# Optimization experiments

Measured on AMD Instinct MI355X. Metric: run time of the kernel, lower is better.

The kernel has to match this reference:

```python
import math
import jax, jax.numpy as jnp
import numpy as np

N_LAYER = 6
THETA = 2.0 ** 16
LN_EPS = 1e-5


def _ln(x):
    # LayerNorm over last dim, no affine (elementwise_affine=False)
    mu = x.mean(-1, keepdims=True)
    var = ((x - mu) ** 2).mean(-1, keepdims=True)
    return (x - mu) / jnp.sqrt(var + LN_EPS)


def _rope(phases, v):
    # phases: (T, N); v: (B, H, T, N)
    ph = (phases % 1.0) * (2.0 * math.pi)
    c, s = jnp.cos(ph), jnp.sin(ph)
    v2 = v.reshape(v.shape[:-1] + (-1, 2))
    v_rot = jnp.stack((-v2[..., 1], v2[..., 0]), axis=-1).reshape(v.shape)
    return v * c + v_rot * s


def setup_inputs() -> dict:
    key = jax.random.key(0)
    ks = jax.random.split(key, 6)
    B, T, D, nh, mult, V = 2, 512, 256, 4, 64, 256
    N = D * mult // nh  # 4096 neurons per head
    std = 0.02
    return {
        "input_ids": jax.random.randint(ks[0], (B, T), 0, V, dtype=jnp.int64),
        "embed_table": jax.random.normal(ks[1], (V, D), jnp.float32) * std,
        "encoder": jax.random.normal(ks[2], (nh, D, N), jnp.float32) * std,
        "encoder_v": jax.random.normal(ks[3], (nh, D, N), jnp.float32) * std,
        "decoder": jax.random.normal(ks[4], (nh * N, D), jnp.float32) * std,
        "lm_head": jax.random.normal(ks[5], (D, V), jnp.float32) * std,
    }


def reference(input_ids, embed_table, encoder, encoder_v, decoder, lm_head):
    B, T = input_ids.shape
    nh, D, N = encoder.shape
    # RoPE freqs: quantize(arange(N), 2) / N exponent (matches get_freqs)
    qidx = jnp.floor(jnp.arange(N, dtype=jnp.float32) / 2.0) * 2.0
    freqs = 1.0 / (THETA ** (qidx / N)) / (2.0 * math.pi)
    phases = jnp.arange(T, dtype=jnp.float32)[:, None] * freqs[None, :]  # (T, N)
    # strictly-lower causal mask (tril with diagonal=-1)
    causal = jnp.tril(jnp.ones((T, T), dtype=bool), k=-1)
    dec = decoder.reshape(nh, N, D)  # head-major, matches transpose(1,2).reshape

    x = _ln(embed_table[input_ids])[:, None]  # (B, 1, T, D)
    trace = None
    for _ in range(N_LAYER):  # shared (tied) weights across layers
        x_sparse = jax.nn.relu(jnp.einsum('bitd,hdn->bhtn', x, encoder))  # (B,H,T,N)
        qr = _rope(phases, x_sparse)
        scores = jnp.einsum('bhtn,bhsn->bhts', qr, qr)  # linear attn, no softmax
        scores = jnp.where(causal, scores, 0.0)
        ykv = _ln(jnp.einsum('bhts,bisd->bhtd', scores, x))  # (B,H,T,D)
        y_sparse = jax.nn.relu(jnp.einsum('bhtd,hdn->bhtn', ykv, encoder_v))
        xy_sparse = x_sparse * y_sparse  # elementwise gate
        trace = xy_sparse  # keep only last layer (used for neuron_trace)
        ymlp = jnp.einsum('bhtn,hnd->btd', xy_sparse, dec)[:, None]  # (B,1,T,D)
        x = _ln(x + _ln(ymlp))

    xs = x[:, 0]  # (B, T, D)
    logits = xs @ lm_head  # (B, T, V)
    embedding = xs.mean(axis=1)  # (B, D), pool_output, no mask
    neuron_trace = trace.mean(axis=2).reshape(B, -1)  # (B, H*N)
    return logits, embedding, neuron_trace
```

## Files before the change

kernel.cpp:

```cpp
#include <hip/hip_runtime.h>
#include <hip/hip_bf16.h>
#include <hip/hip_fp16.h>

#define TT 512
#define DD 256
#define NH 4
#define NN 4096
#define VV 256
#define NLAYER 6
#define BB 2
#define BH (BB * NH)
#define NPAIR 2048

typedef __attribute__((ext_vector_type(8))) short bf16x8;
typedef __attribute__((ext_vector_type(4))) float f32x4;
typedef __attribute__((ext_vector_type(8))) unsigned short us8;
typedef __attribute__((ext_vector_type(4))) unsigned short us4;

#define AS1 __attribute__((address_space(1)))
#define AS3 __attribute__((address_space(3)))

__device__ __forceinline__ void glds16(const unsigned short* g, unsigned short* l) {
  __builtin_amdgcn_global_load_lds((const AS1 void*)g, (AS3 void*)l, 16, 0, 0);
}

__device__ __forceinline__ unsigned short f2bf(float f) {
  unsigned int u = __float_as_uint(f);
  return (unsigned short)((u + 0x7FFFu + ((u >> 16) & 1u)) >> 16);
}
__device__ __forceinline__ float bf2f(unsigned short h) {
  return __uint_as_float((unsigned int)h << 16);
}
__device__ __forceinline__ float h2f(unsigned short h) {
  __half x = *reinterpret_cast<__half*>(&h);
  return __half2float(x);
}

__device__ __forceinline__ float block_sum_256(float v) {
  __shared__ float s[4];
  #pragma unroll
  for (int o = 32; o > 0; o >>= 1) v += __shfl_down(v, o);
  int lane = threadIdx.x & 63, wid = threadIdx.x >> 6;
  if (lane == 0) s[wid] = v;
  __syncthreads();
  float r = s[0] + s[1] + s[2] + s[3];
  __syncthreads();
  return r;
}

__device__ __forceinline__ float wave_sum64(float v) {
  #pragma unroll
  for (int o = 32; o > 0; o >>= 1) v += __shfl_xor(v, o);
  return v;
}

__device__ __forceinline__ void mfma_tile128_w32_dbuf(const unsigned short* __restrict__ A, int lda,
                                                      const unsigned short* __restrict__ B, int ldb,
                                                      int K, f32x4 acc[2][8],
                                                      unsigned short* As, unsigned short* Bs) {
  const int tid = threadIdx.x;
  const int lane = tid & 63, wave = tid >> 6;
  const int fm = lane & 15, fq = lane >> 4;
  const int wrow = wave << 5;
  const int lrow = lane >> 3;
  const int scol = (((lane & 7) ^ lrow) << 3);
  const unsigned short* gA = A + (size_t)(wave * 8 + lrow) * lda + scol;
  const unsigned short* gB = B + (size_t)(wave * 8 + lrow) * ldb + scol;
  const int lbase = wave * 8 * 64;
  const int swz = (fm & 7) << 4;
  #pragma unroll
  for (int i = 0; i < 4; ++i) {
    glds16(gA + (size_t)(i * 32) * lda, As + lbase + i * 32 * 64);
    glds16(gB + (size_t)(i * 32) * ldb, Bs + lbase + i * 32 * 64);
  }
  __syncthreads();
  int cur = 0;
  for (int k0 = 0; k0 < K; k0 += 64) {
    if (k0 + 64 < K) {
      unsigned short* nA = As + (cur ^ 1) * 8192 + lbase;
      unsigned short* nB = Bs + (cur ^ 1) * 8192 + lbase;
      #pragma unroll
      for (int i = 0; i < 4; ++i) {
        glds16(gA + (k0 + 64) + (size_t)(i * 32) * lda, nA + i * 32 * 64);
        glds16(gB + (k0 + 64) + (size_t)(i * 32) * ldb, nB + i * 32 * 64);
      }
    }
    const char* cA = (const char*)(As + cur * 8192);
    const char* cB = (const char*)(Bs + cur * 8192);
    #pragma unroll
    for (int kk = 0; kk < 2; ++kk) {
      bf16x8 af[2], bfv[8];
      #pragma unroll
      for (int i = 0; i < 2; ++i) {
        const int ra = wrow + i * 16 + fm;
        af[i] = *(const bf16x8*)(cA + ((((ra << 7) + (kk << 6) + (fq << 4))) ^ swz));
      }
      #pragma unroll
      for (int i = 0; i < 8; ++i) {
        const int rb = i * 16 + fm;
        bfv[i] = *(const bf16x8*)(cB + ((((rb << 7) + (kk << 6) + (fq << 4))) ^ swz));
      }
      #pragma unroll
      for (int mi = 0; mi < 2; ++mi)
        #pragma unroll
        for (int ni = 0; ni < 8; ++ni)
          acc[mi][ni] = __builtin_amdgcn_mfma_f32_16x16x32_bf16(af[mi], bfv[ni], acc[mi][ni], 0, 0, 0);
    }
    __syncthreads();
    cur ^= 1;
  }
}

__device__ __forceinline__ void mfma_tile128_dbuf(const unsigned short* __restrict__ A, int lda,
                                                  const unsigned short* __restrict__ B, int ldb,
                                                  int K, f32x4 acc[4][4],
                                                  unsigned short* As, unsigned short* Bs) {
  const int tid = threadIdx.x;
  const int lane = tid & 63, wave = tid >> 6;
  const int fm = lane & 15, fq = lane >> 4;
  const int rw = (wave >> 1) << 6, cw = (wave & 1) << 6;
  const int lrow = lane >> 3;
  const int scol = (((lane & 7) ^ lrow) << 3);
  const unsigned short* gA = A + (size_t)(wave * 8 + lrow) * lda + scol;
  const unsigned short* gB = B + (size_t)(wave * 8 + lrow) * ldb + scol;
  const int lbase = wave * 8 * 64;
  const int swz = (fm & 7) << 4;
  #pragma unroll
  for (int i = 0; i < 4; ++i) {
    glds16(gA + (size_t)(i * 32) * lda, As + lbase + i * 32 * 64);
    glds16(gB + (size_t)(i * 32) * ldb, Bs + lbase + i * 32 * 64);
  }
  __syncthreads();
  int cur = 0;
  for (int k0 = 0; k0 < K; k0 += 64) {
    if (k0 + 64 < K) {
      unsigned short* nA = As + (cur ^ 1) * 8192 + lbase;
      unsigned short* nB = Bs + (cur ^ 1) * 8192 + lbase;
      #pragma unroll
      for (int i = 0; i < 4; ++i) {
        glds16(gA + (k0 + 64) + (size_t)(i * 32) * lda, nA + i * 32 * 64);
        glds16(gB + (k0 + 64) + (size_t)(i * 32) * ldb, nB + i * 32 * 64);
      }
    }
    const char* cA = (const char*)(As + cur * 8192);
    const char* cB = (const char*)(Bs + cur * 8192);
    #pragma unroll
    for (int kk = 0; kk < 2; ++kk) {
      bf16x8 af[4], bfv[4];
      #pragma unroll
      for (int i = 0; i < 4; ++i) {
        const int ra = rw + i * 16 + fm;
        const int rb = cw + i * 16 + fm;
        af[i]  = *(const bf16x8*)(cA + ((((ra << 7) + (kk << 6) + (fq << 4))) ^ swz));
        bfv[i] = *(const bf16x8*)(cB + ((((rb << 7) + (kk << 6) + (fq << 4))) ^ swz));
      }
      #pragma unroll
      for (int mi = 0; mi < 4; ++mi)
        #pragma unroll
        for (int ni = 0; ni < 4; ++ni)
          acc[mi][ni] = __builtin_amdgcn_mfma_f32_16x16x32_bf16(af[mi], bfv[ni], acc[mi][ni], 0, 0, 0);
    }
    __syncthreads();
    cur ^= 1;
  }
}


__global__ __launch_bounds__(256) void k_csinit(unsigned int* __restrict__ cs) {
  int idx = blockIdx.x * 256 + threadIdx.x;
  int t = idx >> 11, p = idx & (NPAIR - 1);
  const float INV2PI = 0.15915494309189535f;
  const float TWOPI = 6.283185307179586f;
  float f = exp2f(-16.0f * (float)(2 * p) / (float)NN) * INV2PI;
  float ph = fmodf((float)t * f, 1.0f) * TWOPI;
  float s, c;
  sincosf(ph, &s, &c);
  __half hc = __float2half_rn(c), hs = __float2half_rn(s);
  unsigned short uc = *reinterpret_cast<unsigned short*>(&hc);
  unsigned short us_ = *reinterpret_cast<unsigned short*>(&hs);
  cs[idx] = ((unsigned int)us_ << 16) | uc;
}

__global__ __launch_bounds__(256) void k_tcast(const float* __restrict__ in,
                                               unsigned short* __restrict__ out,
                                               int R, int C) {
  __shared__ float tile[64][65];
  const size_t zoff = (size_t)blockIdx.z * R * C;
  const int r0 = blockIdx.y * 64, c0 = blockIdx.x * 64;
  const int cl = threadIdx.x & 63, r4 = threadIdx.x >> 6;
  #pragma unroll 4
  for (int i = 0; i < 16; ++i) {
    int rl = r4 * 16 + i;
    tile[rl][cl] = in[zoff + (size_t)(r0 + rl) * C + c0 + cl];
  }
  __syncthreads();
  #pragma unroll 4
  for (int i = 0; i < 16; ++i) {
    int ccl = r4 * 16 + i;
    out[zoff + (size_t)(c0 + ccl) * R + r0 + cl] = f2bf(tile[cl][ccl]);
  }
}

__global__ __launch_bounds__(256) void k_embed_ln(const int* __restrict__ idw,
                                                  const float* __restrict__ tbl,
                                                  float* __restrict__ x,
                                                  unsigned short* __restrict__ xbf,
                                                  unsigned short* __restrict__ xTbf) {
  __shared__ int s_id;
  int row = blockIdx.x, tid = threadIdx.x;
  if (tid == 0) {
    bool is64 = true;
    for (int i = 1; i < 64; i += 2)
      if (idw[i] != 0) { is64 = false; break; }
    s_id = is64 ? idw[2 * row] : idw[row];
  }
  __syncthreads();
  int id = s_id;
  float v = tbl[(size_t)id * DD + tid];
  float mu = block_sum_256(v) * (1.0f / DD);
  float d = v - mu;
  float var = block_sum_256(d * d) * (1.0f / DD);
  float r = d * rsqrtf(var + 1e-5f);
  x[(size_t)row * DD + tid] = r;
  unsigned short rb = f2bf(r);
  xbf[(size_t)row * DD + tid] = rb;
  int b = row >> 9, t = row & 511;
  xTbf[((size_t)b * DD + tid) * TT + t] = rb;
}


__global__ __launch_bounds__(256) void k_enc(const unsigned short* __restrict__ xbf,
                                             const unsigned short* __restrict__ encT,
                                             const unsigned int* __restrict__ csh,
                                             unsigned short* __restrict__ xsp,
                                             unsigned short* __restrict__ qr) {
  __shared__ unsigned short smem[32768];
  unsigned short* As = smem;
  unsigned short* Bs = smem + 16384;
  float* smemf = (float*)smem;
  const int tid = threadIdx.x;
  const int lin = blockIdx.x;
  const int bh = lin & 7, r0 = lin >> 3;
  const int b = bh >> 2, h = bh & 3;
  const int m0 = (r0 >> 5) * 128, n0 = (r0 & 31) * 128;
  f32x4 acc[2][8] = {};
  mfma_tile128_w32_dbuf(xbf + (size_t)b * TT * DD + (size_t)m0 * DD, DD,
                        encT + (size_t)h * NN * DD + (size_t)n0 * DD, DD, DD, acc, As, Bs);
  const int lane = tid & 63, wave = tid >> 6;
  const int fm = lane & 15, fq = lane >> 4;
  float* Scw = smemf + wave * (16 * 132);
  const int rr4 = lane >> 4, c0 = (lane & 15) << 3;
  const size_t base = (size_t)bh * TT * NN;
  #pragma unroll
  for (int mi = 0; mi < 2; ++mi) {
    if (mi) asm volatile("s_waitcnt lgkmcnt(0)" ::: "memory");
    #pragma unroll
    for (int ni = 0; ni < 8; ++ni)
      #pragma unroll
      for (int r = 0; r < 4; ++r)
        Scw[(fq * 4 + r) * 132 + ni * 16 + fm] = acc[mi][ni][r];
    asm volatile("s_waitcnt lgkmcnt(0)" ::: "memory");
    #pragma unroll
    for (int k = 0; k < 4; ++k) {
      const int rr = k * 4 + rr4;
      float v[8];
      *(float4*)&v[0] = *(const float4*)&Scw[rr * 132 + c0];
      *(float4*)&v[4] = *(const float4*)&Scw[rr * 132 + c0 + 4];
      const int t = m0 + wave * 32 + mi * 16 + rr;
      const int n = n0 + c0;
      #pragma unroll
      for (int j = 0; j < 8; ++j) v[j] = fmaxf(v[j], 0.0f);
      us8 o;
      #pragma unroll
      for (int j = 0; j < 8; ++j) o[j] = f2bf(v[j]);
      size_t off = base + (size_t)t * NN + n;
      *(us8*)(xsp + off) = o;
      const unsigned short* cp = (const unsigned short*)(csh + (size_t)t * NPAIR + (n >> 1));
      us8 cv = *(const us8*)cp;
      us8 q;
      #pragma unroll
      for (int j = 0; j < 4; ++j) {
        float c = h2f(cv[2 * j]), s = h2f(cv[2 * j + 1]);
        float ve = v[2 * j], vo = v[2 * j + 1];
        q[2 * j]     = f2bf(ve * c - vo * s);
        q[2 * j + 1] = f2bf(vo * c + ve * s);
      }
      *(us8*)(qr + off) = q;
    }
  }
}

__global__ __launch_bounds__(256) void k_scores_part(const unsigned short* __restrict__ qr,
                                                     float* __restrict__ scp) {
  __shared__ float smemf[16384];
  unsigned short* As = (unsigned short*)smemf;
  unsigned short* Bs = As + 16384;
  const int lin = blockIdx.x;
  const int xcd = lin & 7, slot = lin >> 3;
  const int zg = slot / 10, p = slot - zg * 10;
  const int z = xcd * 4 + zg;
  const int bh = z >> 2, kc = z & 3;
  const int mt = (p > 0) + (p > 2) + (p > 5);
  const int nt = p - mt * (mt + 1) / 2;
  const int m0 = mt * 128, n0 = nt * 128;
  const unsigned short* Q = qr + (size_t)bh * TT * NN + kc * 1024;
  f32x4 acc[4][4] = {};
  mfma_tile128_dbuf(Q + (size_t)m0 * NN, NN, Q + (size_t)n0 * NN, NN, 1024, acc, As, Bs);
  const int lane = threadIdx.x & 63, wave = threadIdx.x >> 6;
  const int fm = lane & 15, fq = lane >> 4;
  const int rw = (wave >> 1) << 6, cw = (wave & 1) << 6;
  float* C = scp + (size_t)z * TT * TT;
  const bool diag = (m0 == n0);
  #pragma unroll
  for (int ni = 0; ni < 4; ++ni) {
    int s = n0 + cw + ni * 16 + fm;
    #pragma unroll
    for (int mi = 0; mi < 4; ++mi) {
      int trow = m0 + rw + mi * 16 + (fq << 2);
      #pragma unroll
      for (int r = 0; r < 4; ++r) {
        float v = acc[mi][ni][r];
        if (diag && s >= trow + r) v = 0.0f;
        C[(size_t)(trow + r) * TT + s] = v;
      }
    }
  }
}

__global__ __launch_bounds__(256) void k_ykv_part(const float* __restrict__ scp,
                                                  const unsigned short* __restrict__ xTbf,
                                                  float* __restrict__ ykvp) {
  __shared__ unsigned short As[64][40];
  __shared__ unsigned short Bs[256][40];
  const int tid = threadIdx.x;
  const int lin = blockIdx.x;
  const int bh = lin & 7, r0 = lin >> 3;
  const int m0 = (r0 & 7) * 64, ks = r0 >> 3, b = bh >> 2;
  if (ks * 128 >= m0 + 64) return;
  float* C = ykvp + ((size_t)(bh * 4 + ks) * TT + m0) * DD;
  const int lane = tid & 63, wave = tid >> 6;
  const int srow = tid >> 2, sk = (tid & 3) << 3;
  const int fm = lane & 15, fq = lane >> 4;
  const int t = m0 + srow;
  const size_t abase0 = (size_t)(bh * 4) * TT * TT + (size_t)t * TT;
  const unsigned short* Brow = xTbf + ((size_t)b * DD + tid) * TT + ks * 128;
  f32x4 acc[16] = {};
  for (int k0 = 0; k0 < 128; k0 += 32) {
    const int s0 = ks * 128 + k0 + sk;
    const float* p = scp + abase0 + s0;
    float sum[8];
    float4 u0 = *(const float4*)(p);
    float4 u1 = *(const float4*)(p + 4);
    sum[0] = u0.x; sum[1] = u0.y; sum[2] = u0.z; sum[3] = u0.w;
    sum[4] = u1.x; sum[5] = u1.y; sum[6] = u1.z; sum[7] = u1.w;
    #pragma unroll
    for (int kc = 1; kc < 4; ++kc) {
      float4 v0 = *(const float4*)(p + (size_t)kc * TT * TT);
      float4 v1 = *(const float4*)(p + (size_t)kc * TT * TT + 4);
      sum[0] += v0.x; sum[1] += v0.y; sum[2] += v0.z; sum[3] += v0.w;
      sum[4] += v1.x; sum[5] += v1.y; sum[6] += v1.z; sum[7] += v1.w;
    }
    us8 av;
    #pragma unroll
    for (int j = 0; j < 8; ++j) av[j] = f2bf(sum[j]);
    us8 bv0 = *(const us8*)(Brow + k0);
    us8 bv1 = *(const us8*)(Brow + k0 + 8);
    us8 bv2 = *(const us8*)(Brow + k0 + 16);
    us8 bv3 = *(const us8*)(Brow + k0 + 24);
    __syncthreads();
    *(us8*)(&As[srow][sk]) = av;
    *(us8*)(&Bs[tid][0]) = bv0;
    *(us8*)(&Bs[tid][8]) = bv1;
    *(us8*)(&Bs[tid][16]) = bv2;
    *(us8*)(&Bs[tid][24]) = bv3;
    __syncthreads();
    bf16x8 a = *(const bf16x8*)(&As[wave * 16 + fm][fq << 3]);
    #pragma unroll
    for (int ni = 0; ni < 16; ++ni) {
      bf16x8 bfr = *(const bf16x8*)(&Bs[ni * 16 + fm][fq << 3]);
      acc[ni] = __builtin_amdgcn_mfma_f32_16x16x32_bf16(a, bfr, acc[ni], 0, 0, 0);
    }
  }
  const int trow = wave * 16 + (fq << 2);
  #pragma unroll
  for (int ni = 0; ni < 16; ++ni)
    #pragma unroll
    for (int r = 0; r < 4; ++r)
      C[(size_t)(trow + r) * DD + ni * 16 + fm] = acc[ni][r];
}

__global__ __launch_bounds__(256) void k_ykv_red(const float* __restrict__ ykvp,
                                                 unsigned short* __restrict__ ykvbf) {
  int row = blockIdx.x * 4 + (threadIdx.x >> 6);
  int lane = threadIdx.x & 63;
  int bh = row >> 9, t = row & 511;
  int d0 = lane << 2;
  int nks = (t >> 7) + 1;
  size_t base = ((size_t)(bh * 4) * TT + t) * DD + d0;
  f32x4 v = *(const f32x4*)(ykvp + base);
  if (nks > 1) v += *(const f32x4*)(ykvp + base + (size_t)TT * DD);
  if (nks > 2) v += *(const f32x4*)(ykvp + base + (size_t)2 * TT * DD);
  if (nks > 3) v += *(const f32x4*)(ykvp + base + (size_t)3 * TT * DD);
  float mu = wave_sum64(v.x + v.y + v.z + v.w) * (1.0f / DD);
  f32x4 d = v - mu;
  float var = wave_sum64(d.x * d.x + d.y * d.y + d.z * d.z + d.w * d.w) * (1.0f / DD);
  f32x4 r = d * rsqrtf(var + 1e-5f);
  us4 rb;
  #pragma unroll
  for (int j = 0; j < 4; ++j) rb[j] = f2bf(r[j]);
  *(us4*)(ykvbf + (size_t)row * DD + d0) = rb;
}

__global__ __launch_bounds__(256) void k_ysp_xy(const unsigned short* __restrict__ ykvbf,
                                                const unsigned short* __restrict__ encvT,
                                                const unsigned short* __restrict__ xsp,
                                                unsigned short* __restrict__ xy) {
  __shared__ unsigned short smem[32768];
  unsigned short* As = smem;
  unsigned short* Bs = smem + 16384;
  float* smemf = (float*)smem;
  const int tid = threadIdx.x;
  const int lin = blockIdx.x;
  const int bh = lin & 7, r0 = lin >> 3;
  const int h = bh & 3;
  const int m0 = (r0 >> 5) * 128, n0 = (r0 & 31) * 128;
  f32x4 acc[2][8] = {};
  mfma_tile128_w32_dbuf(ykvbf + (size_t)bh * TT * DD + (size_t)m0 * DD, DD,
                        encvT + (size_t)h * NN * DD + (size_t)n0 * DD, DD, DD, acc, As, Bs);
  const int lane = tid & 63, wave = tid >> 6;
  const int fm = lane & 15, fq = lane >> 4;
  float* Scw = smemf + wave * (16 * 132);
  const int rr4 = lane >> 4, c0 = (lane & 15) << 3;
  const size_t base = (size_t)bh * TT * NN;
  #pragma unroll
  for (int mi = 0; mi < 2; ++mi) {
    if (mi) asm volatile("s_waitcnt lgkmcnt(0)" ::: "memory");
    #pragma unroll
    for (int ni = 0; ni < 8; ++ni)
      #pragma unroll
      for (int r = 0; r < 4; ++r)
        Scw[(fq * 4 + r) * 132 + ni * 16 + fm] = acc[mi][ni][r];
    asm volatile("s_waitcnt lgkmcnt(0)" ::: "memory");
    #pragma unroll
    for (int k = 0; k < 4; ++k) {
      const int rr = k * 4 + rr4;
      float v[8];
      *(float4*)&v[0] = *(const float4*)&Scw[rr * 132 + c0];
      *(float4*)&v[4] = *(const float4*)&Scw[rr * 132 + c0 + 4];
      const int t = m0 + wave * 32 + mi * 16 + rr;
      const int n = n0 + c0;
      size_t off = base + (size_t)t * NN + n;
      us8 x0 = *(const us8*)(xsp + off);
      us8 o;
      #pragma unroll
      for (int j = 0; j < 8; ++j)
        o[j] = f2bf(bf2f(x0[j]) * fmaxf(v[j], 0.0f));
      *(us8*)(xy + off) = o;
    }
  }
}

__global__ __launch_bounds__(256) void k_ymlp(const unsigned short* __restrict__ xy,
                                              const unsigned short* __restrict__ decT,
                                              float* __restrict__ ym32) {
  __shared__ float smemf[16384];
  unsigned short* As = (unsigned short*)smemf;
  unsigned short* Bs = As + 16384;
  const int lin = blockIdx.x;
  const int xcd = lin & 7, r0 = lin >> 3;
  const int z = xcd * 8 + (r0 >> 3);
  const int tile = r0 & 7;
  const int bh = z >> 3, ks = z & 7, h = bh & 3;
  const int m0 = (tile & 3) * 128, n0 = (tile >> 2) * 128;
  f32x4 acc[4][4] = {};
  mfma_tile128_dbuf(xy + (size_t)bh * TT * NN + (size_t)m0 * NN + ks * 512, NN,
                    decT + (size_t)h * DD * NN + (size_t)n0 * NN + ks * 512, NN,
                    512, acc, As, Bs);
  const int lane = threadIdx.x & 63, wave = threadIdx.x >> 6;
  const int fm = lane & 15, fq = lane >> 4;
  const int rw = (wave >> 1) << 6, cw = (wave & 1) << 6;
  float* C = ym32 + (size_t)z * TT * DD;
  #pragma unroll
  for (int ni = 0; ni < 4; ++ni) {
    int d = n0 + cw + ni * 16 + fm;
    #pragma unroll
    for (int mi = 0; mi < 4; ++mi) {
      int trow = m0 + rw + mi * 16 + (fq << 2);
      #pragma unroll
      for (int r = 0; r < 4; ++r)
        C[(size_t)(trow + r) * DD + d] = acc[mi][ni][r];
    }
  }
}

__global__ __launch_bounds__(256) void k_ln2(float* __restrict__ x,
                                             const float* __restrict__ ym32,
                                             unsigned short* __restrict__ xbf,
                                             unsigned short* __restrict__ xTbf) {
  int row = blockIdx.x * 4 + (threadIdx.x >> 6);
  int lane = threadIdx.x & 63;
  int b = row >> 9, t = row & 511;
  int d0 = lane << 2;
  f32x4 y = {0.0f, 0.0f, 0.0f, 0.0f};
  size_t rbase = (size_t)t * DD + d0;
  #pragma unroll
  for (int p = 0; p < 32; ++p)
    y += *(const f32x4*)(ym32 + (size_t)(b * 32 + p) * TT * DD + rbase);
  float mu = wave_sum64(y.x + y.y + y.z + y.w) * (1.0f / DD);
  f32x4 d = y - mu;
  float var = wave_sum64(d.x * d.x + d.y * d.y + d.z * d.z + d.w * d.w) * (1.0f / DD);
  f32x4 ly = d * rsqrtf(var + 1e-5f);
  f32x4 xv = *(const f32x4*)(x + (size_t)row * DD + d0) + ly;
  float mu2 = wave_sum64(xv.x + xv.y + xv.z + xv.w) * (1.0f / DD);
  f32x4 d2 = xv - mu2;
  float var2 = wave_sum64(d2.x * d2.x + d2.y * d2.y + d2.z * d2.z + d2.w * d2.w) * (1.0f / DD);
  f32x4 r = d2 * rsqrtf(var2 + 1e-5f);
  *(f32x4*)(x + (size_t)row * DD + d0) = r;
  us4 rb;
  #pragma unroll
  for (int j = 0; j < 4; ++j) rb[j] = f2bf(r[j]);
  *(us4*)(xbf + (size_t)row * DD + d0) = rb;
  #pragma unroll
  for (int j = 0; j < 4; ++j)
    xTbf[((size_t)b * DD + d0 + j) * TT + t] = rb[j];
}

__global__ __launch_bounds__(256) void k_trace_part(const unsigned short* __restrict__ xy,
                                                    float* __restrict__ part) {
  const int lin = blockIdx.x;
  const int ts = lin & 7, nc = (lin >> 3) & 1, bh = lin >> 4;
  const int n0 = nc * 2048 + threadIdx.x * 8;
  const size_t base = (size_t)bh * TT * NN + n0;
  float acc[8];
  #pragma unroll
  for (int j = 0; j < 8; ++j) acc[j] = 0.0f;
  for (int t = ts * 64; t < ts * 64 + 64; ++t) {
    us8 v = *(const us8*)(xy + base + (size_t)t * NN);
    #pragma unroll
    for (int j = 0; j < 8; ++j) acc[j] += bf2f(v[j]);
  }
  float* o = part + (size_t)(bh * 8 + ts) * NN + n0;
  #pragma unroll
  for (int j = 0; j < 8; ++j) o[j] = acc[j];
}

__global__ __launch_bounds__(256) void k_trace_red(const float* __restrict__ part,
                                                   float* __restrict__ out) {
  int idx = blockIdx.x * 256 + threadIdx.x;
  int bh = idx >> 12, n = idx & 4095;
  float s = 0.0f;
  #pragma unroll
  for (int ts = 0; ts < 8; ++ts)
    s += part[(size_t)(bh * 8 + ts) * NN + n];
  out[idx] = s * (1.0f / TT);
}

__global__ __launch_bounds__(256) void k_logits(const float* __restrict__ x,
                                                const float* __restrict__ W,
                                                float* __restrict__ out) {
  __shared__ float xs[DD];
  int row = blockIdx.x, tid = threadIdx.x;
  xs[tid] = x[(size_t)row * DD + tid];
  __syncthreads();
  float s = 0.0f;
  #pragma unroll 8
  for (int d = 0; d < DD; ++d) s = fmaf(xs[d], W[(size_t)d * VV + tid], s);
  out[(size_t)row * VV + tid] = s;
}

__global__ __launch_bounds__(256) void k_embedding(const float* __restrict__ x,
                                                   float* __restrict__ out) {
  int idx = blockIdx.x * 256 + threadIdx.x;
  int b = idx >> 8, d = idx & 255;
  float s = 0.0f;
  for (int t = 0; t < TT; ++t) s += x[(size_t)(b * TT + t) * DD + d];
  out[idx] = s * (1.0f / TT);
}

extern "C" void kernel_launch(void* const* d_in, const int* in_sizes, int n_in,
                              void* d_out, int out_size, void* d_ws, size_t ws_size,
                              hipStream_t stream) {
  const int*   ids  = (const int*)d_in[0];
  const float* tbl  = (const float*)d_in[1];
  const float* enc  = (const float*)d_in[2];
  const float* encv = (const float*)d_in[3];
  const float* dec  = (const float*)d_in[4];
  const float* lmh  = (const float*)d_in[5];

  float* ws   = (float*)d_ws;
  float* x    = ws;
  unsigned short* ykvbf = (unsigned short*)(x + 262144);
  float* ym32 = (float*)(ykvbf + 1048576);
  unsigned short* xbf   = (unsigned short*)(ym32 + 8388608);
  unsigned short* xTbf  = xbf + 262144;
  unsigned short* encT  = xTbf + 262144;
  unsigned short* encvT = encT + 4194304;
  unsigned short* decT  = encvT + 4194304;
  unsigned short* xspbf = decT + 4194304;
  unsigned short* qxybf = xspbf + 16777216;
  unsigned int* cs = (unsigned int*)(qxybf + 16777216);
  float* scp  = (float*)(cs + 2097152);
  float* ykvp = scp + 8388608;

  float* out_logits = (float*)d_out;
  float* out_embed  = out_logits + (size_t)BB * TT * VV;
  float* out_trace  = out_embed + (size_t)BB * DD;

  k_csinit<<<(TT * NPAIR) / 256, 256, 0, stream>>>(cs);
  k_tcast<<<dim3(NN / 64, DD / 64, NH), 256, 0, stream>>>(enc,  encT,  DD, NN);
  k_tcast<<<dim3(NN / 64, DD / 64, NH), 256, 0, stream>>>(encv, encvT, DD, NN);
  k_tcast<<<dim3(DD / 64, NN / 64, NH), 256, 0, stream>>>(dec,  decT,  NN, DD);

  k_embed_ln<<<BB * TT, 256, 0, stream>>>(ids, tbl, x, xbf, xTbf);
  for (int l = 0; l < NLAYER; ++l) {
    k_enc        <<<1024, 256, 0, stream>>>(xbf, encT, cs, xspbf, qxybf);
    k_scores_part<<<320, 256, 0, stream>>>(qxybf, scp);
    k_ykv_part   <<<256, 256, 0, stream>>>(scp, xTbf, ykvp);
    k_ykv_red    <<<BH * TT / 4, 256, 0, stream>>>(ykvp, ykvbf);
    k_ysp_xy     <<<1024, 256, 0, stream>>>(ykvbf, encvT, xspbf, qxybf);
    k_ymlp       <<<512, 256, 0, stream>>>(qxybf, decT, ym32);
    k_ln2        <<<BB * TT / 4, 256, 0, stream>>>(x, ym32, xbf, xTbf);
  }
  k_trace_part<<<128, 256, 0, stream>>>(qxybf, scp);
  k_trace_red <<<128, 256, 0, stream>>>(scp, out_trace);
  k_logits    <<<BB * TT, 256, 0, stream>>>(x, lmh, out_logits);
  k_embedding <<<(BB * DD) / 256, 256, 0, stream>>>(x, out_embed);
}
```

Measured before the change: 741.2 us.

## Pipeline GEMM tile loads with vmcnt waits, retile ykv_part, halve ymlp split-K

The shared double-buffered MFMA tile loops now issue the next stage's global-to-LDS loads and wait only on the previous stage using s_waitcnt vmcnt plus raw s_barrier, instead of full __syncthreads. This lets loads overlap with compute. k_ykv_part is restructured to stage a full 128-wide K chunk of reduced scores and xT into LDS once, with 32-row tiles and twice the blocks, which removes the per-32-K-step sync loop. k_ymlp moves from 8 to 4 split-K partitions with K=1024 each, halving partial writes and the ln2 reduction, but launching fewer blocks.

```diff
diff --git a/kernel.cpp b/kernel.cpp
--- a/kernel.cpp
+++ b/kernel.cpp
@@ -66,14 +66,13 @@
   const int scol = (((lane & 7) ^ lrow) << 3);
   const unsigned short* gA = A + (size_t)(wave * 8 + lrow) * lda + scol;
   const unsigned short* gB = B + (size_t)(wave * 8 + lrow) * ldb + scol;
-  const int lbase = wave * 8 * 64;
+  const int lbase = wave * 512;
   const int swz = (fm & 7) << 4;
   #pragma unroll
   for (int i = 0; i < 4; ++i) {
-    glds16(gA + (size_t)(i * 32) * lda, As + lbase + i * 32 * 64);
-    glds16(gB + (size_t)(i * 32) * ldb, Bs + lbase + i * 32 * 64);
-  }
-  __syncthreads();
+    glds16(gA + (size_t)(i * 32) * lda, As + lbase + i * 2048);
+    glds16(gB + (size_t)(i * 32) * ldb, Bs + lbase + i * 2048);
+  }
   int cur = 0;
   for (int k0 = 0; k0 < K; k0 += 64) {
     if (k0 + 64 < K) {
@@ -81,10 +80,15 @@
       unsigned short* nB = Bs + (cur ^ 1) * 8192 + lbase;
       #pragma unroll
       for (int i = 0; i < 4; ++i) {
-        glds16(gA + (k0 + 64) + (size_t)(i * 32) * lda, nA + i * 32 * 64);
-        glds16(gB + (k0 + 64) + (size_t)(i * 32) * ldb, nB + i * 32 * 64);
-      }
-    }
+        glds16(gA + (k0 + 64) + (size_t)(i * 32) * lda, nA + i * 2048);
+        glds16(gB + (k0 + 64) + (size_t)(i * 32) * ldb, nB + i * 2048);
+      }
+      asm volatile("s_waitcnt vmcnt(8)" ::: "memory");
+    } else {
+      asm volatile("s_waitcnt vmcnt(0)" ::: "memory");
+    }
+    __builtin_amdgcn_s_barrier();
+    __builtin_amdgcn_sched_barrier(0);
     const char* cA = (const char*)(As + cur * 8192);
     const char* cB = (const char*)(Bs + cur * 8192);
     #pragma unroll
@@ -106,7 +110,8 @@
         for (int ni = 0; ni < 8; ++ni)
           acc[mi][ni] = __builtin_amdgcn_mfma_f32_16x16x32_bf16(af[mi], bfv[ni], acc[mi][ni], 0, 0, 0);
     }
-    __syncthreads();
+    __builtin_amdgcn_sched_barrier(0);
+    __builtin_amdgcn_s_barrier();
     cur ^= 1;
   }
 }
@@ -123,14 +128,13 @@
   const int scol = (((lane & 7) ^ lrow) << 3);
   const unsigned short* gA = A + (size_t)(wave * 8 + lrow) * lda + scol;
   const unsigned short* gB = B + (size_t)(wave * 8 + lrow) * ldb + scol;
-  const int lbase = wave * 8 * 64;
+  const int lbase = wave * 512;
   const int swz = (fm & 7) << 4;
   #pragma unroll
   for (int i = 0; i < 4; ++i) {
-    glds16(gA + (size_t)(i * 32) * lda, As + lbase + i * 32 * 64);
-    glds16(gB + (size_t)(i * 32) * ldb, Bs + lbase + i * 32 * 64);
-  }
-  __syncthreads();
+    glds16(gA + (size_t)(i * 32) * lda, As + lbase + i * 2048);
+    glds16(gB + (size_t)(i * 32) * ldb, Bs + lbase + i * 2048);
+  }
   int cur = 0;
   for (int k0 = 0; k0 < K; k0 += 64) {
     if (k0 + 64 < K) {
@@ -138,10 +142,15 @@
       unsigned short* nB = Bs + (cur ^ 1) * 8192 + lbase;
       #pragma unroll
       for (int i = 0; i < 4; ++i) {
-        glds16(gA + (k0 + 64) + (size_t)(i * 32) * lda, nA + i * 32 * 64);
-        glds16(gB + (k0 + 64) + (size_t)(i * 32) * ldb, nB + i * 32 * 64);
-      }
-    }
+        glds16(gA + (k0 + 64) + (size_t)(i * 32) * lda, nA + i * 2048);
+        glds16(gB + (k0 + 64) + (size_t)(i * 32) * ldb, nB + i * 2048);
+      }
+      asm volatile("s_waitcnt vmcnt(8)" ::: "memory");
+    } else {
+      asm volatile("s_waitcnt vmcnt(0)" ::: "memory");
+    }
+    __builtin_amdgcn_s_barrier();
+    __builtin_amdgcn_sched_barrier(0);
     const char* cA = (const char*)(As + cur * 8192);
     const char* cB = (const char*)(Bs + cur * 8192);
     #pragma unroll
@@ -160,7 +169,8 @@
         for (int ni = 0; ni < 4; ++ni)
           acc[mi][ni] = __builtin_amdgcn_mfma_f32_16x16x32_bf16(af[mi], bfv[ni], acc[mi][ni], 0, 0, 0);
     }
-    __syncthreads();
+    __builtin_amdgcn_sched_barrier(0);
+    __builtin_amdgcn_s_barrier();
     cur ^= 1;
   }
 }
@@ -330,63 +340,70 @@
 __global__ __launch_bounds__(256) void k_ykv_part(const float* __restrict__ scp,
                                                   const unsigned short* __restrict__ xTbf,
                                                   float* __restrict__ ykvp) {
-  __shared__ unsigned short As[64][40];
-  __shared__ unsigned short Bs[256][40];
+  __shared__ unsigned short As[32][136];
+  __shared__ unsigned short Bs[256][136];
   const int tid = threadIdx.x;
   const int lin = blockIdx.x;
   const int bh = lin & 7, r0 = lin >> 3;
-  const int m0 = (r0 & 7) * 64, ks = r0 >> 3, b = bh >> 2;
-  if (ks * 128 >= m0 + 64) return;
+  const int jp = r0 & 15, ks = r0 >> 4, b = bh >> 2;
+  const int m0 = jp * 32;
+  if (ks * 128 >= m0 + 32) return;
   float* C = ykvp + ((size_t)(bh * 4 + ks) * TT + m0) * DD;
+  {
+    const int srow = tid >> 3;
+    const int sk = (tid & 7) << 4;
+    const float* p0 = scp + (size_t)(bh * 4) * TT * TT + (size_t)(m0 + srow) * TT + ks * 128 + sk;
+    #pragma unroll
+    for (int oc = 0; oc < 2; ++oc) {
+      const float* p = p0 + oc * 8;
+      float sum[8];
+      float4 u0 = *(const float4*)(p);
+      float4 u1 = *(const float4*)(p + 4);
+      sum[0] = u0.x; sum[1] = u0.y; sum[2] = u0.z; sum[3] = u0.w;
+      sum[4] = u1.x; sum[5] = u1.y; sum[6] = u1.z; sum[7] = u1.w;
+      #pragma unroll
+      for (int kc = 1; kc < 4; ++kc) {
+        float4 v0 = *(const float4*)(p + (size_t)kc * TT * TT);
+        float4 v1 = *(const float4*)(p + (size_t)kc * TT * TT + 4);
+        sum[0] += v0.x; sum[1] += v0.y; sum[2] += v0.z; sum[3] += v0.w;
+        sum[4] += v1.x; sum[5] += v1.y; sum[6] += v1.z; sum[7] += v1.w;
+      }
+      us8 av;
+      #pragma unroll
+      for (int j = 0; j < 8; ++j) av[j] = f2bf(sum[j]);
+      *(us8*)(&As[srow][sk + oc * 8]) = av;
+    }
+  }
+  {
+    const unsigned short* Brow = xTbf + ((size_t)b * DD + tid) * TT + ks * 128;
+    #pragma unroll
+    for (int i = 0; i < 16; ++i) {
+      us8 v = *(const us8*)(Brow + i * 8);
+      *(us8*)(&Bs[tid][i * 8]) = v;
+    }
+  }
+  __syncthreads();
   const int lane = tid & 63, wave = tid >> 6;
-  const int srow = tid >> 2, sk = (tid & 3) << 3;
   const int fm = lane & 15, fq = lane >> 4;
-  const int t = m0 + srow;
-  const size_t abase0 = (size_t)(bh * 4) * TT * TT + (size_t)t * TT;
-  const unsigned short* Brow = xTbf + ((size_t)b * DD + tid) * TT + ks * 128;
-  f32x4 acc[16] = {};
-  for (int k0 = 0; k0 < 128; k0 += 32) {
-    const int s0 = ks * 128 + k0 + sk;
-    const float* p = scp + abase0 + s0;
-    float sum[8];
-    float4 u0 = *(const float4*)(p);
-    float4 u1 = *(const float4*)(p + 4);
-    sum[0] = u0.x; sum[1] = u0.y; sum[2] = u0.z; sum[3] = u0.w;
-    sum[4] = u1.x; sum[5] = u1.y; sum[6] = u1.z; sum[7] = u1.w;
-    #pragma unroll
-    for (int kc = 1; kc < 4; ++kc) {
-      float4 v0 = *(const float4*)(p + (size_t)kc * TT * TT);
-      float4 v1 = *(const float4*)(p + (size_t)kc * TT * TT + 4);
-      sum[0] += v0.x; sum[1] += v0.y; sum[2] += v0.z; sum[3] += v0.w;
-      sum[4] += v1.x; sum[5] += v1.y; sum[6] += v1.z; sum[7] += v1.w;
-    }
-    us8 av;
-    #pragma unroll
-    for (int j = 0; j < 8; ++j) av[j] = f2bf(sum[j]);
-    us8 bv0 = *(const us8*)(Brow + k0);
-    us8 bv1 = *(const us8*)(Brow + k0 + 8);
-    us8 bv2 = *(const us8*)(Brow + k0 + 16);
-    us8 bv3 = *(const us8*)(Brow + k0 + 24);
-    __syncthreads();
-    *(us8*)(&As[srow][sk]) = av;
-    *(us8*)(&Bs[tid][0]) = bv0;
-    *(us8*)(&Bs[tid][8]) = bv1;
-    *(us8*)(&Bs[tid][16]) = bv2;
-    *(us8*)(&Bs[tid][24]) = bv3;
-    __syncthreads();
-    bf16x8 a = *(const bf16x8*)(&As[wave * 16 + fm][fq << 3]);
-    #pragma unroll
-    for (int ni = 0; ni < 16; ++ni) {
-      bf16x8 bfr = *(const bf16x8*)(&Bs[ni * 16 + fm][fq << 3]);
-      acc[ni] = __builtin_amdgcn_mfma_f32_16x16x32_bf16(a, bfr, acc[ni], 0, 0, 0);
-    }
-  }
-  const int trow = wave * 16 + (fq << 2);
-  #pragma unroll
-  for (int ni = 0; ni < 16; ++ni)
+  const int mf = wave & 1, cfb = (wave >> 1) * 8;
+  bf16x8 a[4];
+  #pragma unroll
+  for (int kk = 0; kk < 4; ++kk)
+    a[kk] = *(const bf16x8*)(&As[mf * 16 + fm][kk * 32 + (fq << 3)]);
+  f32x4 acc[8] = {};
+  #pragma unroll
+  for (int ni = 0; ni < 8; ++ni)
+    #pragma unroll
+    for (int kk = 0; kk < 4; ++kk) {
+      bf16x8 bv = *(const bf16x8*)(&Bs[(cfb + ni) * 16 + fm][kk * 32 + (fq << 3)]);
+      acc[ni] = __builtin_amdgcn_mfma_f32_16x16x32_bf16(a[kk], bv, acc[ni], 0, 0, 0);
+    }
+  const int trow = mf * 16 + (fq << 2);
+  #pragma unroll
+  for (int ni = 0; ni < 8; ++ni)
     #pragma unroll
     for (int r = 0; r < 4; ++r)
-      C[(size_t)(trow + r) * DD + ni * 16 + fm] = acc[ni][r];
+      C[(size_t)(trow + r) * DD + (cfb + ni) * 16 + fm] = acc[ni][r];
 }
 
 __global__ __launch_bounds__(256) void k_ykv_red(const float* __restrict__ ykvp,
@@ -467,15 +484,14 @@
   unsigned short* As = (unsigned short*)smemf;
   unsigned short* Bs = As + 16384;
   const int lin = blockIdx.x;
-  const int xcd = lin & 7, r0 = lin >> 3;
-  const int z = xcd * 8 + (r0 >> 3);
-  const int tile = r0 & 7;
-  const int bh = z >> 3, ks = z & 7, h = bh & 3;
+  const int bh = lin & 7, r0 = lin >> 3;
+  const int ks = r0 >> 3, tile = r0 & 7;
+  const int z = bh * 4 + ks, h = bh & 3;
   const int m0 = (tile & 3) * 128, n0 = (tile >> 2) * 128;
   f32x4 acc[4][4] = {};
-  mfma_tile128_dbuf(xy + (size_t)bh * TT * NN + (size_t)m0 * NN + ks * 512, NN,
-                    decT + (size_t)h * DD * NN + (size_t)n0 * NN + ks * 512, NN,
-                    512, acc, As, Bs);
+  mfma_tile128_dbuf(xy + (size_t)bh * TT * NN + (size_t)m0 * NN + ks * 1024, NN,
+                    decT + (size_t)h * DD * NN + (size_t)n0 * NN + ks * 1024, NN,
+                    1024, acc, As, Bs);
   const int lane = threadIdx.x & 63, wave = threadIdx.x >> 6;
   const int fm = lane & 15, fq = lane >> 4;
   const int rw = (wave >> 1) << 6, cw = (wave & 1) << 6;
@@ -504,8 +520,8 @@
   f32x4 y = {0.0f, 0.0f, 0.0f, 0.0f};
   size_t rbase = (size_t)t * DD + d0;
   #pragma unroll
-  for (int p = 0; p < 32; ++p)
-    y += *(const f32x4*)(ym32 + (size_t)(b * 32 + p) * TT * DD + rbase);
+  for (int p = 0; p < 16; ++p)
+    y += *(const f32x4*)(ym32 + (size_t)(b * 16 + p) * TT * DD + rbase);
   float mu = wave_sum64(y.x + y.y + y.z + y.w) * (1.0f / DD);
   f32x4 d = y - mu;
   float var = wave_sum64(d.x * d.x + d.y * d.y + d.z * d.z + d.w * d.w) * (1.0f / DD);
@@ -615,10 +631,10 @@
   for (int l = 0; l < NLAYER; ++l) {
     k_enc        <<<1024, 256, 0, stream>>>(xbf, encT, cs, xspbf, qxybf);
     k_scores_part<<<320, 256, 0, stream>>>(qxybf, scp);
-    k_ykv_part   <<<256, 256, 0, stream>>>(scp, xTbf, ykvp);
+    k_ykv_part   <<<512, 256, 0, stream>>>(scp, xTbf, ykvp);
     k_ykv_red    <<<BH * TT / 4, 256, 0, stream>>>(ykvp, ykvbf);
     k_ysp_xy     <<<1024, 256, 0, stream>>>(ykvbf, encvT, xspbf, qxybf);
-    k_ymlp       <<<512, 256, 0, stream>>>(qxybf, decT, ym32);
+    k_ymlp       <<<256, 256, 0, stream>>>(qxybf, decT, ym32);
     k_ln2        <<<BB * TT / 4, 256, 0, stream>>>(x, ym32, xbf, xTbf);
   }
   k_trace_part<<<128, 256, 0, stream>>>(qxybf, scp);
```

Result: slower. 781.7 us (+5.5%).
